# Kernel tuning notes

Measured on AMD Instinct MI355X. Metric: run time of the kernel, lower is better.

Reference implementation:

```python
import jax, jax.numpy as jnp
import numpy as np

D_MODEL = 1024
D_HEAD = 64
B, S = 4, 2048


def setup_inputs() -> dict:
    key = jax.random.key(0)
    ks = jax.random.split(key, 4)
    scale = 1.0 / np.sqrt(D_MODEL)
    return {
        "embeddings": jax.random.normal(ks[0], (B, S, D_MODEL), dtype=jnp.float32),
        "Wq": jax.random.normal(ks[1], (D_MODEL, D_HEAD), dtype=jnp.float32) * scale,
        "bq": jnp.zeros((D_HEAD,), dtype=jnp.float32),
        "Wk": jax.random.normal(ks[2], (D_MODEL, D_HEAD), dtype=jnp.float32) * scale,
        "bk": jnp.zeros((D_HEAD,), dtype=jnp.float32),
        "Wv": jax.random.normal(ks[3], (D_MODEL, D_HEAD), dtype=jnp.float32) * scale,
        "bv": jnp.zeros((D_HEAD,), dtype=jnp.float32),
    }


def reference(embeddings, Wq, bq, Wk, bk, Wv, bv):
    # Q, K, V projections: (b, s, d_head)
    Q = embeddings @ Wq + bq
    K = embeddings @ Wk + bk
    V = embeddings @ Wv + bv
    # scaled scores: (b, s, s)
    scores = jnp.einsum("bqd,bkd->bqk", Q, K) / jnp.sqrt(jnp.float32(D_HEAD))
    # causal mask: positions k > q get -inf
    s = scores.shape[-1]
    causal = jnp.tril(jnp.ones((s, s), dtype=bool))
    scores = jnp.where(causal, scores, -jnp.inf)
    pattern = jax.nn.softmax(scores, axis=-1)
    # attention output: (b, s, d_head)  (note: original forward skips self.output)
    return jnp.einsum("bqk,bkd->bqd", pattern, V)
```

## Files before the change

kernel.cpp:

```cpp
#include <hip/hip_runtime.h>
#include <hip/hip_bf16.h>

#define DMODEL 1024
#define DH 64
#define BB 4
#define SS 2048
#define NROW (BB * SS)
#define NS 8

typedef __attribute__((ext_vector_type(8))) short bf16x8;
typedef __attribute__((ext_vector_type(4))) float f32x4;

__device__ __forceinline__ unsigned short f2bf(float f) {
    __hip_bfloat16 h = __float2bfloat16(f);
    return __builtin_bit_cast(unsigned short, h);
}
__device__ __forceinline__ float bf2f(unsigned short u) {
    unsigned v = (unsigned)u << 16;
    return __builtin_bit_cast(float, v);
}

__global__ __launch_bounds__(256) void prep_wt_kernel(
    const float* __restrict__ Wq, const float* __restrict__ Wk,
    const float* __restrict__ Wv, unsigned short* __restrict__ Wt)
{
    __shared__ float T[64][65];
    const int tid = threadIdx.x;
    const int m   = blockIdx.x;
    const int k0  = blockIdx.y * 64;
    const float* W = (m == 0) ? Wq : (m == 1) ? Wk : Wv;

    const int tn = tid & 63, tk = tid >> 6;
    #pragma unroll
    for (int j = 0; j < 16; ++j)
        T[4 * j + tk][tn] = W[(size_t)(k0 + 4 * j + tk) * DH + tn];
    __syncthreads();

    const int wk = tid & 63, wn = tid >> 6;
    #pragma unroll
    for (int j = 0; j < 16; ++j)
        Wt[(size_t)(m * 64 + 4 * j + wn) * DMODEL + k0 + wk] =
            f2bf(T[wk][4 * j + wn]);
}

__global__ __launch_bounds__(256) void qkv_proj_mfma(
    const float* __restrict__ emb, const unsigned short* __restrict__ Wt,
    const float* __restrict__ bq, const float* __restrict__ bk,
    const float* __restrict__ bv,
    unsigned short* __restrict__ Q, unsigned short* __restrict__ K,
    unsigned short* __restrict__ V)
{
    __shared__ unsigned short Bs[2][96][256];

    const int tid  = threadIdx.x;
    const int lane = tid & 63;
    const int w    = tid >> 6;
    const int c    = lane & 15;
    const int g    = lane >> 4;
    const int row0    = blockIdx.x * 64;
    const int colbase = blockIdx.y * 96;

    const float* arow = emb + (size_t)(row0 + 16 * w + c) * DMODEL + 8 * g;

    f32x4 acc[6];
    #pragma unroll
    for (int t = 0; t < 6; ++t) acc[t] = (f32x4){0.f, 0.f, 0.f, 0.f};

    float4 aR[4][4];

    const int lrow_off = lane >> 5;
    const int lslot    = lane & 31;

#define ISSUEB(QTR, BI) do {                                                  \
    _Pragma("unroll")                                                         \
    for (int j = 0; j < 12; ++j) {                                            \
        const int rb = 24 * w + 2 * j;                                        \
        const int rr = rb + lrow_off;                                         \
        __builtin_amdgcn_global_load_lds(                                     \
            (const __attribute__((address_space(1))) void*)(                  \
                Wt + (size_t)(colbase + rr) * DMODEL + (QTR) * 256            \
                   + 8 * (lslot ^ (rr & 7))),                                 \
            (__attribute__((address_space(3))) void*)&Bs[BI][rb][0],          \
            16, 0, 0);                                                        \
    }                                                                         \
} while (0)

#define LOADA(S, R) do {                                                      \
    aR[R][0] = *reinterpret_cast<const float4*>(arow + 64 * (S));             \
    aR[R][1] = *reinterpret_cast<const float4*>(arow + 64 * (S) + 4);         \
    aR[R][2] = *reinterpret_cast<const float4*>(arow + 64 * (S) + 32);        \
    aR[R][3] = *reinterpret_cast<const float4*>(arow + 64 * (S) + 36);        \
} while (0)

    ISSUEB(0, 0);
    LOADA(0, 0);
    LOADA(1, 1);
    LOADA(2, 2);
    asm volatile("s_waitcnt vmcnt(12)" ::: "memory");
    __builtin_amdgcn_sched_barrier(0);
    __syncthreads();

    #pragma unroll
    for (int q = 0; q < 4; ++q) {
        const int bi = q & 1;
        if (q < 3) ISSUEB(q + 1, bi ^ 1);

        #pragma unroll
        for (int s2 = 0; s2 < 4; ++s2) {
            const int S = 4 * q + s2;
            const int r = S & 3;
            if (S + 3 < 16) LOADA(S + 3, (S + 3) & 3);

            bf16x8 af[2];
            {
                union { bf16x8 v; unsigned short u[8]; } p0, p1;
                p0.u[0] = f2bf(aR[r][0].x); p0.u[1] = f2bf(aR[r][0].y);
                p0.u[2] = f2bf(aR[r][0].z); p0.u[3] = f2bf(aR[r][0].w);
                p0.u[4] = f2bf(aR[r][1].x); p0.u[5] = f2bf(aR[r][1].y);
                p0.u[6] = f2bf(aR[r][1].z); p0.u[7] = f2bf(aR[r][1].w);
                p1.u[0] = f2bf(aR[r][2].x); p1.u[1] = f2bf(aR[r][2].y);
                p1.u[2] = f2bf(aR[r][2].z); p1.u[3] = f2bf(aR[r][2].w);
                p1.u[4] = f2bf(aR[r][3].x); p1.u[5] = f2bf(aR[r][3].y);
                p1.u[6] = f2bf(aR[r][3].z); p1.u[7] = f2bf(aR[r][3].w);
                af[0] = p0.v; af[1] = p1.v;
            }

            #pragma unroll
            for (int t = 0; t < 6; ++t)
                #pragma unroll
                for (int kp = 0; kp < 2; ++kp) {
                    const int row  = 16 * t + c;
                    const int slot = (8 * s2 + 4 * kp + g) ^ (row & 7);
                    bf16x8 bfr = __builtin_bit_cast(bf16x8,
                        *reinterpret_cast<const uint4*>(&Bs[bi][row][slot * 8]));
                    acc[t] = __builtin_amdgcn_mfma_f32_16x16x32_bf16(
                        af[kp], bfr, acc[t], 0, 0, 0);
                }
        }
        if (q < 3) {
            asm volatile("s_waitcnt vmcnt(12)" ::: "memory");
            __builtin_amdgcn_sched_barrier(0);
            __syncthreads();
        }
    }
#undef ISSUEB
#undef LOADA

    #pragma unroll
    for (int t = 0; t < 6; ++t) {
        const int col = colbase + 16 * t + c;
        const int m   = col >> 6;
        const int lc  = col & 63;
        const float* bias = (m == 0) ? bq : (m == 1) ? bk : bv;
        unsigned short* O = (m == 0) ? Q : (m == 1) ? K : V;
        const float bs    = bias[lc];
        const float scale = (m == 0) ? 0.125f : 1.0f;
        #pragma unroll
        for (int i = 0; i < 4; ++i) {
            const int rr = row0 + 16 * w + 4 * g + i;
            O[(size_t)rr * DH + lc] = f2bf((acc[t][i] + bs) * scale);
        }
    }
}

__global__ __launch_bounds__(512) void attn_mfma_split(
    const unsigned short* __restrict__ Q, const unsigned short* __restrict__ K,
    const unsigned short* __restrict__ V,
    unsigned short* __restrict__ Opart, float* __restrict__ mpart,
    float* __restrict__ lpart)
{
    __shared__ unsigned short Ks[64][72];
    __shared__ unsigned short Vt[64][72];
    __shared__ unsigned short Ps[8][16][72];

    const int tid  = threadIdx.x;
    const int lane = tid & 63;
    const int w    = tid >> 6;
    const int c    = lane & 15;
    const int g    = lane >> 4;
    const int qt   = blockIdx.x;
    const int b    = blockIdx.y;
    const int sp   = blockIdx.z;
    const int q0   = qt * 128;

    const int ntile = 2 * qt + 2;
    const int kt0 = (ntile * sp) / NS;
    const int kt1 = (ntile * (sp + 1)) / NS;

    const unsigned short* Qb = Q + (size_t)b * SS * DH;
    const unsigned short* Kb = K + (size_t)b * SS * DH;
    const unsigned short* Vb = V + (size_t)b * SS * DH;

    bf16x8 qa[2];
    #pragma unroll
    for (int kp = 0; kp < 2; ++kp)
        qa[kp] = __builtin_bit_cast(bf16x8,
            *reinterpret_cast<const uint4*>(
                &Qb[(size_t)(q0 + 16 * w + c) * DH + 32 * kp + 8 * g]));

    f32x4 o[4];
    #pragma unroll
    for (int t = 0; t < 4; ++t) o[t] = (f32x4){0.f, 0.f, 0.f, 0.f};
    float m_i = -1e30f;
    float l_i = 0.f;

    const int kvs = tid >> 3;
    const int m8  = tid & 7;
    const int d0  = m8 * 8;

    for (int kt = kt0; kt < kt1; ++kt) {
        const int kb0 = kt * 64;
        __syncthreads();
        {
            *reinterpret_cast<uint4*>(&Ks[kvs][d0]) =
                *reinterpret_cast<const uint4*>(&Kb[(size_t)(kb0 + kvs) * DH + d0]);
            const uint4 vv =
                *reinterpret_cast<const uint4*>(&Vb[(size_t)(kb0 + kvs) * DH + d0]);
            const unsigned wd[4] = {vv.x, vv.y, vv.z, vv.w};
            #pragma unroll
            for (int e = 0; e < 8; ++e)
                Vt[(d0 + e) ^ m8][kvs] =
                    (unsigned short)(wd[e >> 1] >> (16 * (e & 1)));
        }
        __syncthreads();

        f32x4 s[4];
        #pragma unroll
        for (int t = 0; t < 4; ++t) s[t] = (f32x4){0.f, 0.f, 0.f, 0.f};
        #pragma unroll
        for (int t = 0; t < 4; ++t)
            #pragma unroll
            for (int kp = 0; kp < 2; ++kp) {
                bf16x8 kf = __builtin_bit_cast(bf16x8,
                    *reinterpret_cast<const uint4*>(&Ks[16 * t + c][32 * kp + 8 * g]));
                s[t] = __builtin_amdgcn_mfma_f32_16x16x32_bf16(kf, qa[kp], s[t], 0, 0, 0);
            }

        if (kt >= 2 * qt) {
            const int qg = q0 + 16 * w + c;
            #pragma unroll
            for (int t = 0; t < 4; ++t)
                #pragma unroll
                for (int i = 0; i < 4; ++i)
                    if (kb0 + 16 * t + 4 * g + i > qg) s[t][i] = -1e30f;
        }

        float mx = m_i;
        #pragma unroll
        for (int t = 0; t < 4; ++t)
            mx = fmaxf(mx, fmaxf(fmaxf(s[t][0], s[t][1]), fmaxf(s[t][2], s[t][3])));
        mx = fmaxf(mx, __shfl_xor(mx, 16));
        mx = fmaxf(mx, __shfl_xor(mx, 32));
        const float al = __expf(m_i - mx);
        m_i = mx;
        float sum = 0.f;
        #pragma unroll
        for (int t = 0; t < 4; ++t)
            #pragma unroll
            for (int i = 0; i < 4; ++i) {
                const float p = __expf(s[t][i] - mx);
                s[t][i] = p;
                sum += p;
            }
        sum += __shfl_xor(sum, 16);
        sum += __shfl_xor(sum, 32);
        l_i = l_i * al + sum;

        #pragma unroll
        for (int t = 0; t < 4; ++t) {
            uint2 u;
            u.x = (unsigned)f2bf(s[t][0]) | ((unsigned)f2bf(s[t][1]) << 16);
            u.y = (unsigned)f2bf(s[t][2]) | ((unsigned)f2bf(s[t][3]) << 16);
            *reinterpret_cast<uint2*>(&Ps[w][c][16 * t + 4 * g]) = u;
        }

        #pragma unroll
        for (int t = 0; t < 4; ++t)
            #pragma unroll
            for (int i = 0; i < 4; ++i)
                o[t][i] *= al;

        #pragma unroll
        for (int kp = 0; kp < 2; ++kp) {
            bf16x8 pb = __builtin_bit_cast(bf16x8,
                *reinterpret_cast<const uint4*>(&Ps[w][c][32 * kp + 8 * g]));
            #pragma unroll
            for (int t = 0; t < 4; ++t) {
                const int dv = 16 * t + c;
                const int pr = dv ^ ((2 * t + (c >> 3)) & 7);
                bf16x8 vf = __builtin_bit_cast(bf16x8,
                    *reinterpret_cast<const uint4*>(&Vt[pr][32 * kp + 8 * g]));
                o[t] = __builtin_amdgcn_mfma_f32_16x16x32_bf16(vf, pb, o[t], 0, 0, 0);
            }
        }
    }

    const int qrow = b * SS + q0 + 16 * w + c;
    #pragma unroll
    for (int t = 0; t < 4; ++t) {
        uint2 u;
        u.x = (unsigned)f2bf(o[t][0]) | ((unsigned)f2bf(o[t][1]) << 16);
        u.y = (unsigned)f2bf(o[t][2]) | ((unsigned)f2bf(o[t][3]) << 16);
        *reinterpret_cast<uint2*>(
            &Opart[((size_t)sp * NROW + qrow) * DH + 16 * t + 4 * g]) = u;
    }
    if (g == 0) {
        mpart[(size_t)sp * NROW + qrow] = m_i;
        lpart[(size_t)sp * NROW + qrow] = l_i;
    }
}

__global__ __launch_bounds__(256) void attn_combine(
    const unsigned short* __restrict__ Opart, const float* __restrict__ mpart,
    const float* __restrict__ lpart, float* __restrict__ out)
{
    const int idx = blockIdx.x * 256 + threadIdx.x;
    const int row = idx >> 4;
    const int d4  = (idx & 15) * 4;

    float m[NS];
    float M = -1e30f;
    #pragma unroll
    for (int s = 0; s < NS; ++s) {
        m[s] = mpart[(size_t)s * NROW + row];
        M = fmaxf(M, m[s]);
    }
    float L = 0.f;
    float4 acc = {0.f, 0.f, 0.f, 0.f};
    #pragma unroll
    for (int s = 0; s < NS; ++s) {
        const float wgt = __expf(m[s] - M);
        L += wgt * lpart[(size_t)s * NROW + row];
        const uint2 pu = *reinterpret_cast<const uint2*>(
            &Opart[((size_t)s * NROW + row) * DH + d4]);
        acc.x += wgt * bf2f((unsigned short)(pu.x & 0xffff));
        acc.y += wgt * bf2f((unsigned short)(pu.x >> 16));
        acc.z += wgt * bf2f((unsigned short)(pu.y & 0xffff));
        acc.w += wgt * bf2f((unsigned short)(pu.y >> 16));
    }
    const float inv = 1.f / L;
    float4 r = {acc.x * inv, acc.y * inv, acc.z * inv, acc.w * inv};
    *reinterpret_cast<float4*>(&out[(size_t)row * DH + d4]) = r;
}

extern "C" void kernel_launch(void* const* d_in, const int* in_sizes, int n_in,
                              void* d_out, int out_size, void* d_ws, size_t ws_size,
                              hipStream_t stream) {
    const float* emb = (const float*)d_in[0];
    const float* Wq  = (const float*)d_in[1];
    const float* bq  = (const float*)d_in[2];
    const float* Wk  = (const float*)d_in[3];
    const float* bk  = (const float*)d_in[4];
    const float* Wv  = (const float*)d_in[5];
    const float* bv  = (const float*)d_in[6];
    float* out = (float*)d_out;

    unsigned short* Qw = (unsigned short*)d_ws;
    unsigned short* Kw = Qw + (size_t)NROW * DH;
    unsigned short* Vw = Kw + (size_t)NROW * DH;
    unsigned short* Wt = Vw + (size_t)NROW * DH;
    unsigned short* Opart = Wt + (size_t)192 * DMODEL;
    float* mpart = (float*)(Opart + (size_t)NS * NROW * DH);
    float* lpart = mpart + (size_t)NS * NROW;

    hipLaunchKernelGGL(prep_wt_kernel, dim3(3, 16), dim3(256), 0, stream,
                       Wq, Wk, Wv, Wt);
    hipLaunchKernelGGL(qkv_proj_mfma, dim3(NROW / 64, 2), dim3(256), 0, stream,
                       emb, Wt, bq, bk, bv, Qw, Kw, Vw);
    hipLaunchKernelGGL(attn_mfma_split, dim3(SS / 128, BB, NS), dim3(512), 0, stream,
                       Qw, Kw, Vw, Opart, mpart, lpart);
    hipLaunchKernelGGL(attn_combine, dim3(NROW * 16 / 256), dim3(256), 0, stream,
                       Opart, mpart, lpart, out);
}
```

Before: 42.78 us.

## Process two 128-row query halves per attention block to reuse K/V tiles

Each split-KV attention block now handles 256 query rows as two 128-row halves, sharing each K/V tile loaded into LDS across both. Per-half causal skipping avoids computing on tiles beyond a half's diagonal. This is meant to halve K/V global and LDS staging traffic per query. In exchange the grid shrinks to half as many blocks, and register pressure grows from the doubled accumulators and Q fragments, which may lower occupancy and worsen load balance.

```diff
diff --git a/kernel.cpp b/kernel.cpp
--- a/kernel.cpp
+++ b/kernel.cpp
@@ -181,9 +181,9 @@
     const int qt   = blockIdx.x;
     const int b    = blockIdx.y;
     const int sp   = blockIdx.z;
-    const int q0   = qt * 128;
-
-    const int ntile = 2 * qt + 2;
+    const int q0   = qt * 256;
+
+    const int ntile = 4 * qt + 4;
     const int kt0 = (ntile * sp) / NS;
     const int kt1 = (ntile * (sp + 1)) / NS;
 
@@ -191,18 +191,22 @@
     const unsigned short* Kb = K + (size_t)b * SS * DH;
     const unsigned short* Vb = V + (size_t)b * SS * DH;
 
-    bf16x8 qa[2];
-    #pragma unroll
-    for (int kp = 0; kp < 2; ++kp)
-        qa[kp] = __builtin_bit_cast(bf16x8,
-            *reinterpret_cast<const uint4*>(
-                &Qb[(size_t)(q0 + 16 * w + c) * DH + 32 * kp + 8 * g]));
-
-    f32x4 o[4];
-    #pragma unroll
-    for (int t = 0; t < 4; ++t) o[t] = (f32x4){0.f, 0.f, 0.f, 0.f};
-    float m_i = -1e30f;
-    float l_i = 0.f;
+    bf16x8 qa[2][2];
+    #pragma unroll
+    for (int h = 0; h < 2; ++h)
+        #pragma unroll
+        for (int kp = 0; kp < 2; ++kp)
+            qa[h][kp] = __builtin_bit_cast(bf16x8,
+                *reinterpret_cast<const uint4*>(
+                    &Qb[(size_t)(q0 + 128 * h + 16 * w + c) * DH + 32 * kp + 8 * g]));
+
+    f32x4 o[2][4];
+    #pragma unroll
+    for (int h = 0; h < 2; ++h)
+        #pragma unroll
+        for (int t = 0; t < 4; ++t) o[h][t] = (f32x4){0.f, 0.f, 0.f, 0.f};
+    float m_i[2] = {-1e30f, -1e30f};
+    float l_i[2] = {0.f, 0.f};
 
     const int kvs = tid >> 3;
     const int m8  = tid & 7;
@@ -224,89 +228,102 @@
         }
         __syncthreads();
 
-        f32x4 s[4];
-        #pragma unroll
-        for (int t = 0; t < 4; ++t) s[t] = (f32x4){0.f, 0.f, 0.f, 0.f};
-        #pragma unroll
-        for (int t = 0; t < 4; ++t)
+        #pragma unroll
+        for (int h = 0; h < 2; ++h) {
+            const int qbase = q0 + 128 * h;
+            if (kb0 > qbase + 127) continue;
+
+            f32x4 s[4];
+            #pragma unroll
+            for (int t = 0; t < 4; ++t) s[t] = (f32x4){0.f, 0.f, 0.f, 0.f};
+            #pragma unroll
+            for (int t = 0; t < 4; ++t)
+                #pragma unroll
+                for (int kp = 0; kp < 2; ++kp) {
+                    bf16x8 kf = __builtin_bit_cast(bf16x8,
+                        *reinterpret_cast<const uint4*>(
+                            &Ks[16 * t + c][32 * kp + 8 * g]));
+                    s[t] = __builtin_amdgcn_mfma_f32_16x16x32_bf16(
+                        kf, qa[h][kp], s[t], 0, 0, 0);
+                }
+
+            if (kb0 >= qbase) {
+                const int qg = qbase + 16 * w + c;
+                #pragma unroll
+                for (int t = 0; t < 4; ++t)
+                    #pragma unroll
+                    for (int i = 0; i < 4; ++i)
+                        if (kb0 + 16 * t + 4 * g + i > qg) s[t][i] = -1e30f;
+            }
+
+            float mx = m_i[h];
+            #pragma unroll
+            for (int t = 0; t < 4; ++t)
+                mx = fmaxf(mx, fmaxf(fmaxf(s[t][0], s[t][1]),
+                                     fmaxf(s[t][2], s[t][3])));
+            mx = fmaxf(mx, __shfl_xor(mx, 16));
+            mx = fmaxf(mx, __shfl_xor(mx, 32));
+            const float al = __expf(m_i[h] - mx);
+            m_i[h] = mx;
+            float sum = 0.f;
+            #pragma unroll
+            for (int t = 0; t < 4; ++t)
+                #pragma unroll
+                for (int i = 0; i < 4; ++i) {
+                    const float p = __expf(s[t][i] - mx);
+                    s[t][i] = p;
+                    sum += p;
+                }
+            sum += __shfl_xor(sum, 16);
+            sum += __shfl_xor(sum, 32);
+            l_i[h] = l_i[h] * al + sum;
+
+            #pragma unroll
+            for (int t = 0; t < 4; ++t) {
+                uint2 u;
+                u.x = (unsigned)f2bf(s[t][0]) | ((unsigned)f2bf(s[t][1]) << 16);
+                u.y = (unsigned)f2bf(s[t][2]) | ((unsigned)f2bf(s[t][3]) << 16);
+                *reinterpret_cast<uint2*>(&Ps[w][c][16 * t + 4 * g]) = u;
+            }
+
+            #pragma unroll
+            for (int t = 0; t < 4; ++t)
+                #pragma unroll
+                for (int i = 0; i < 4; ++i)
+                    o[h][t][i] *= al;
+
             #pragma unroll
             for (int kp = 0; kp < 2; ++kp) {
-                bf16x8 kf = __builtin_bit_cast(bf16x8,
-                    *reinterpret_cast<const uint4*>(&Ks[16 * t + c][32 * kp + 8 * g]));
-                s[t] = __builtin_amdgcn_mfma_f32_16x16x32_bf16(kf, qa[kp], s[t], 0, 0, 0);
+                bf16x8 pb = __builtin_bit_cast(bf16x8,
+                    *reinterpret_cast<const uint4*>(&Ps[w][c][32 * kp + 8 * g]));
+                #pragma unroll
+                for (int t = 0; t < 4; ++t) {
+                    const int dv = 16 * t + c;
+                    const int pr = dv ^ ((2 * t + (c >> 3)) & 7);
+                    bf16x8 vf = __builtin_bit_cast(bf16x8,
+                        *reinterpret_cast<const uint4*>(&Vt[pr][32 * kp + 8 * g]));
+                    o[h][t] = __builtin_amdgcn_mfma_f32_16x16x32_bf16(
+                        vf, pb, o[h][t], 0, 0, 0);
+                }
             }
-
-        if (kt >= 2 * qt) {
-            const int qg = q0 + 16 * w + c;
-            #pragma unroll
-            for (int t = 0; t < 4; ++t)
-                #pragma unroll
-                for (int i = 0; i < 4; ++i)
-                    if (kb0 + 16 * t + 4 * g + i > qg) s[t][i] = -1e30f;
-        }
-
-        float mx = m_i;
-        #pragma unroll
-        for (int t = 0; t < 4; ++t)
-            mx = fmaxf(mx, fmaxf(fmaxf(s[t][0], s[t][1]), fmaxf(s[t][2], s[t][3])));
-        mx = fmaxf(mx, __shfl_xor(mx, 16));
-        mx = fmaxf(mx, __shfl_xor(mx, 32));
-        const float al = __expf(m_i - mx);
-        m_i = mx;
-        float sum = 0.f;
-        #pragma unroll
-        for (int t = 0; t < 4; ++t)
-            #pragma unroll
-            for (int i = 0; i < 4; ++i) {
-                const float p = __expf(s[t][i] - mx);
-                s[t][i] = p;
-                sum += p;
-            }
-        sum += __shfl_xor(sum, 16);
-        sum += __shfl_xor(sum, 32);
-        l_i = l_i * al + sum;
-
+        }
+    }
+
+    #pragma unroll
+    for (int h = 0; h < 2; ++h) {
+        const int qrow = b * SS + q0 + 128 * h + 16 * w + c;
         #pragma unroll
         for (int t = 0; t < 4; ++t) {
             uint2 u;
-            u.x = (unsigned)f2bf(s[t][0]) | ((unsigned)f2bf(s[t][1]) << 16);
-            u.y = (unsigned)f2bf(s[t][2]) | ((unsigned)f2bf(s[t][3]) << 16);
-            *reinterpret_cast<uint2*>(&Ps[w][c][16 * t + 4 * g]) = u;
-        }
-
-        #pragma unroll
-        for (int t = 0; t < 4; ++t)
-            #pragma unroll
-            for (int i = 0; i < 4; ++i)
-                o[t][i] *= al;
-
-        #pragma unroll
-        for (int kp = 0; kp < 2; ++kp) {
-            bf16x8 pb = __builtin_bit_cast(bf16x8,
-                *reinterpret_cast<const uint4*>(&Ps[w][c][32 * kp + 8 * g]));
-            #pragma unroll
-            for (int t = 0; t < 4; ++t) {
-                const int dv = 16 * t + c;
-                const int pr = dv ^ ((2 * t + (c >> 3)) & 7);
-                bf16x8 vf = __builtin_bit_cast(bf16x8,
-                    *reinterpret_cast<const uint4*>(&Vt[pr][32 * kp + 8 * g]));
-                o[t] = __builtin_amdgcn_mfma_f32_16x16x32_bf16(vf, pb, o[t], 0, 0, 0);
-            }
-        }
-    }
-
-    const int qrow = b * SS + q0 + 16 * w + c;
-    #pragma unroll
-    for (int t = 0; t < 4; ++t) {
-        uint2 u;
-        u.x = (unsigned)f2bf(o[t][0]) | ((unsigned)f2bf(o[t][1]) << 16);
-        u.y = (unsigned)f2bf(o[t][2]) | ((unsigned)f2bf(o[t][3]) << 16);
-        *reinterpret_cast<uint2*>(
-            &Opart[((size_t)sp * NROW + qrow) * DH + 16 * t + 4 * g]) = u;
-    }
-    if (g == 0) {
-        mpart[(size_t)sp * NROW + qrow] = m_i;
-        lpart[(size_t)sp * NROW + qrow] = l_i;
+            u.x = (unsigned)f2bf(o[h][t][0]) | ((unsigned)f2bf(o[h][t][1]) << 16);
+            u.y = (unsigned)f2bf(o[h][t][2]) | ((unsigned)f2bf(o[h][t][3]) << 16);
+            *reinterpret_cast<uint2*>(
+                &Opart[((size_t)sp * NROW + qrow) * DH + 16 * t + 4 * g]) = u;
+        }
+        if (g == 0) {
+            mpart[(size_t)sp * NROW + qrow] = m_i[h];
+            lpart[(size_t)sp * NROW + qrow] = l_i[h];
+        }
     }
 }
 
@@ -367,7 +384,7 @@
                        Wq, Wk, Wv, Wt);
     hipLaunchKernelGGL(qkv_proj_mfma, dim3(NROW / 64, 2), dim3(256), 0, stream,
                        emb, Wt, bq, bk, bv, Qw, Kw, Vw);
-    hipLaunchKernelGGL(attn_mfma_split, dim3(SS / 128, BB, NS), dim3(512), 0, stream,
+    hipLaunchKernelGGL(attn_mfma_split, dim3(SS / 256, BB, NS), dim3(512), 0, stream,
                        Qw, Kw, Vw, Opart, mpart, lpart);
     hipLaunchKernelGGL(attn_combine, dim3(NROW * 16 / 256), dim3(256), 0, stream,
                        Opart, mpart, lpart, out);
```

New measurement: 43.82 us. 2.4% more time.
